# Performance work log

Measured on AMD Instinct MI355X. Metric: run time of the kernel, lower is better.

Reference implementation:

```python
import math
import jax, jax.numpy as jnp
import numpy as np

DIM = 1536
HEADS = 8
DK = 64
DV = 192
NRPF = 192  # num_rel_pos_features, divisible by 6
SEQ = 1536
BATCH = 4
SCALE = DK ** -0.5


def get_positional_embed(n, feature_size):
    # distances in [-(n-1), n-1], length 2n-1
    dist = jnp.arange(-n + 1, n).astype(jnp.float32)
    adist = jnp.abs(dist)[:, None]  # [2n-1, 1]
    f = feature_size // 6  # 3 feature fns, each doubled by sign channel
    # exponential half-life features
    max_range = math.log(n) / math.log(2.0)
    half_life = 2.0 ** jnp.linspace(3.0, max_range, f)[None, :]
    emb_exp = jnp.exp(-math.log(2.0) / half_life * adist)
    # central mask features
    center_widths = (2.0 ** jnp.arange(1, f + 1).astype(jnp.float32) - 1.0)[None, :]
    emb_cm = (center_widths > adist).astype(jnp.float32)
    # gamma pdf features
    stddev = n / (2.0 * f)
    start_mean = n / float(f)
    mean = jnp.linspace(start_mean, float(n), f)[None, :]
    conc = (mean / stddev) ** 2
    rate = mean / stddev ** 2
    log_unnorm = (conc - 1.0) * jnp.log(jnp.maximum(adist, 1e-20)) - rate * adist
    log_norm = jax.scipy.special.gammaln(conc) - conc * jnp.log(rate)
    prob = jnp.exp(log_unnorm - log_norm) + 1e-8
    emb_g = prob / jnp.max(prob, axis=-1, keepdims=True)
    emb = jnp.concatenate([emb_exp, emb_cm, emb_g], axis=-1)  # [2n-1, feat/2]
    return jnp.concatenate([emb, jnp.sign(dist)[:, None] * emb], axis=-1)  # [2n-1, feat]


def relative_shift(x):
    # x: [b, h, n, 2n-1] -> [b, h, n, n] via the Transformer-XL shift trick
    b, h, t1, t2 = x.shape
    x = jnp.concatenate([jnp.zeros_like(x[..., :1]), x], axis=-1)  # [b,h,t1,t2+1]
    x = x.reshape(b, h, t2 + 1, t1)[:, :, 1:, :].reshape(b, h, t1, t2)
    return x[..., : (t2 + 2) // 2]


def layer_norm(x, g, b, eps=1e-5):
    mu = jnp.mean(x, axis=-1, keepdims=True)
    var = jnp.var(x, axis=-1, keepdims=True)
    return (x - mu) * jax.lax.rsqrt(var + eps) * g + b


def setup_inputs() -> dict:
    key = jax.random.key(0)
    ks = jax.random.split(key, 16)
    d, h, dk, dv = DIM, HEADS, DK, DV
    inp = {
        "x": jax.random.normal(ks[0], (BATCH, SEQ, d), dtype=jnp.float32),
        "ln1_g": jnp.ones((d,), jnp.float32),
        "ln1_b": jnp.zeros((d,), jnp.float32),
        "Wq": jax.random.normal(ks[1], (d, h * dk), jnp.float32) / math.sqrt(d),
        "Wk": jax.random.normal(ks[2], (d, h * dk), jnp.float32) / math.sqrt(d),
        "Wv": jax.random.normal(ks[3], (d, h * dv), jnp.float32) / math.sqrt(d),
        "Wo": jax.random.normal(ks[4], (h * dv, d), jnp.float32) / math.sqrt(h * dv),
        "bo": jnp.zeros((d,), jnp.float32),
        "Wrk": jax.random.normal(ks[5], (NRPF, h * dk), jnp.float32) / math.sqrt(NRPF),
        "rel_content_bias": jax.random.normal(ks[6], (1, h, 1, dk), jnp.float32),
        "rel_pos_bias": jax.random.normal(ks[7], (1, h, 1, dk), jnp.float32),
        "ln2_g": jnp.ones((d,), jnp.float32),
        "ln2_b": jnp.zeros((d,), jnp.float32),
        "W1": jax.random.normal(ks[8], (d, 2 * d), jnp.float32) / math.sqrt(d),
        "b1": jnp.zeros((2 * d,), jnp.float32),
        "W2": jax.random.normal(ks[9], (2 * d, d), jnp.float32) / math.sqrt(2 * d),
        "b2": jnp.zeros((d,), jnp.float32),
    }
    return inp


def _attention(x, Wq, Wk, Wv, Wo, bo, Wrk, rel_content_bias, rel_pos_bias):
    b, n, _ = x.shape
    h, dk, dv = HEADS, DK, DV
    q = (x @ Wq).reshape(b, n, h, dk).transpose(0, 2, 1, 3) * SCALE  # [b,h,n,dk]
    k = (x @ Wk).reshape(b, n, h, dk).transpose(0, 2, 1, 3)
    v = (x @ Wv).reshape(b, n, h, dv).transpose(0, 2, 1, 3)
    content_logits = jnp.einsum('bhid,bhjd->bhij', q + rel_content_bias, k)
    positions = get_positional_embed(n, NRPF)  # [2n-1, NRPF]
    rel_k = (positions @ Wrk).reshape(2 * n - 1, h, dk).transpose(1, 0, 2)  # [h,2n-1,dk]
    rel_logits = jnp.einsum('bhid,hjd->bhij', q + rel_pos_bias, rel_k)
    rel_logits = relative_shift(rel_logits)  # [b,h,n,n]
    attn = jax.nn.softmax(content_logits + rel_logits, axis=-1)
    out = jnp.einsum('bhij,bhjd->bhid', attn, v)
    out = out.transpose(0, 2, 1, 3).reshape(b, n, h * dv)
    return out @ Wo + bo


def reference(x, ln1_g, ln1_b, Wq, Wk, Wv, Wo, bo, Wrk, rel_content_bias,
              rel_pos_bias, ln2_g, ln2_b, W1, b1, W2, b2):
    # pre-LN attention with residual
    x = x + _attention(layer_norm(x, ln1_g, ln1_b), Wq, Wk, Wv, Wo, bo, Wrk,
                       rel_content_bias, rel_pos_bias)
    # MLP block (carries its own LayerNorm and residual)
    y = layer_norm(x, ln2_g, ln2_b)
    y = jax.nn.relu(y @ W1 + b1)
    y = y @ W2 + b2
    return y + x
```

## Files before the change

### kernel.cpp

```cpp
#include <hip/hip_runtime.h>
#include <hip/hip_bf16.h>
#include <math.h>

#define SEQN 1536
#define NH 8
#define MROWS 6144
#define NDIST 3071

typedef __attribute__((ext_vector_type(8))) _Float16 f16x8;
typedef __attribute__((ext_vector_type(4))) _Float16 f16x4;
typedef __attribute__((ext_vector_type(4))) float f32x4;

#define MFMAH(a, b, c) __builtin_amdgcn_mfma_f32_16x16x32_f16(a, b, c, 0, 0, 0)

__device__ __forceinline__ void gl_lds16(const void* g, void* l) {
  __builtin_amdgcn_global_load_lds(
      (const __attribute__((address_space(1))) void*)g,
      (__attribute__((address_space(3))) void*)l, 16, 0, 0);
}

__global__ __launch_bounds__(64) void pos_embed_kernel(float* __restrict__ pos) {
  int row = blockIdx.x;
  int j = threadIdx.x;
  if (j >= 32) return;
  float dist = (float)(row - (SEQN - 1));
  float adist = fabsf(dist);
  float sgn = (dist > 0.f) ? 1.f : (dist < 0.f ? -1.f : 0.f);

  const float max_range = 10.58496250072116f;
  float hl = exp2f(3.0f + ((max_range - 3.0f) / 31.0f) * (float)j);
  float e_exp = expf(-0.6931471805599453f / hl * adist);

  float cw = exp2f((float)(j + 1)) - 1.0f;
  float e_cm = (cw > adist) ? 1.0f : 0.0f;

  float mean = 48.0f * (float)(j + 1);
  float tt = mean / 24.0f;
  float conc = tt * tt;
  float rate = mean / 576.0f;
  float log_unnorm = (conc - 1.0f) * logf(fmaxf(adist, 1e-20f)) - rate * adist;
  float log_norm = lgammaf(conc) - conc * logf(rate);
  float prob = expf(log_unnorm - log_norm) + 1e-8f;
  float mx = prob;
  #pragma unroll
  for (int off = 16; off >= 1; off >>= 1)
    mx = fmaxf(mx, __shfl_xor(mx, off, 32));
  float e_g = prob / mx;

  float* o = pos + (size_t)row * 192;
  o[j] = e_exp;        o[32 + j] = e_cm;        o[64 + j] = e_g;
  o[96 + j] = sgn * e_exp; o[128 + j] = sgn * e_cm; o[160 + j] = sgn * e_g;
}

__global__ __launch_bounds__(512) void relk_kernel(
    const float* __restrict__ pos, const float* __restrict__ Wrk,
    const float* __restrict__ pb, _Float16* __restrict__ rk, float* __restrict__ PR) {
  __shared__ float prow[16][192];
  const int d0 = blockIdx.x * 16;
  const int t = threadIdx.x;
  #pragma unroll
  for (int p = 0; p < 6; ++p) {
    int idx = t + p * 512;
    int r = idx / 192, c = idx - r * 192;
    prow[r][c] = pos[(size_t)(d0 + r) * 192 + c];
  }
  __syncthreads();
  float acc[16];
  #pragma unroll
  for (int r = 0; r < 16; ++r) acc[r] = 0.f;
  #pragma unroll 4
  for (int kk = 0; kk < 192; ++kk) {
    float wv = Wrk[(size_t)kk * 512 + t];
    #pragma unroll
    for (int r = 0; r < 16; ++r) acc[r] = fmaf(prow[r][kk], wv, acc[r]);
  }
  #pragma unroll
  for (int r = 0; r < 16; ++r)
    rk[(size_t)(d0 + r) * 512 + t] = (_Float16)acc[r];
  float pbv = pb[t];
  #pragma unroll
  for (int r = 0; r < 16; ++r) {
    float pv = pbv * acc[r];
    #pragma unroll
    for (int off = 32; off >= 1; off >>= 1) pv += __shfl_xor(pv, off);
    if ((t & 63) == 0 && (d0 + r) < NDIST)
      PR[(size_t)(t >> 6) * NDIST + d0 + r] = pv;
  }
}

__global__ __launch_bounds__(256) void ck_kernel(
    const _Float16* __restrict__ Kp, const float* __restrict__ cb,
    float* __restrict__ CK) {
  const int gid = blockIdx.x * 4 + (threadIdx.x >> 6);
  const int lane = threadIdx.x & 63;
  const int row = gid >> 3;
  const int h = gid & 7;
  float kv = (float)Kp[(size_t)row * 512 + h * 64 + lane];
  float pv = cb[h * 64 + lane] * kv;
  #pragma unroll
  for (int off = 32; off >= 1; off >>= 1) pv += __shfl_xor(pv, off);
  if (lane == 0) CK[(size_t)row * 8 + h] = pv;
}

__global__ __launch_bounds__(256) void ln_kernel(
    const float* __restrict__ x, const float* __restrict__ g,
    const float* __restrict__ bta, _Float16* __restrict__ oh) {
  const int row = blockIdx.x;
  const int t = threadIdx.x;
  __shared__ float red[4];
  __shared__ float bc[2];
  const float4* xr = (const float4*)(x + (size_t)row * 1536);
  float4 v0 = xr[t];
  float4 v1 = make_float4(0.f, 0.f, 0.f, 0.f);
  if (t < 128) v1 = xr[256 + t];
  float s = v0.x + v0.y + v0.z + v0.w;
  if (t < 128) s += v1.x + v1.y + v1.z + v1.w;
  #pragma unroll
  for (int off = 32; off >= 1; off >>= 1) s += __shfl_xor(s, off);
  if ((t & 63) == 0) red[t >> 6] = s;
  __syncthreads();
  if (t == 0) bc[0] = (red[0] + red[1] + red[2] + red[3]) * (1.f / 1536.f);
  __syncthreads();
  const float mu = bc[0];
  float d, s2 = 0.f;
  d = v0.x - mu; s2 += d * d; d = v0.y - mu; s2 += d * d;
  d = v0.z - mu; s2 += d * d; d = v0.w - mu; s2 += d * d;
  if (t < 128) {
    d = v1.x - mu; s2 += d * d; d = v1.y - mu; s2 += d * d;
    d = v1.z - mu; s2 += d * d; d = v1.w - mu; s2 += d * d;
  }
  #pragma unroll
  for (int off = 32; off >= 1; off >>= 1) s2 += __shfl_xor(s2, off);
  if ((t & 63) == 0) red[t >> 6] = s2;
  __syncthreads();
  if (t == 0) bc[1] = (red[0] + red[1] + red[2] + red[3]) * (1.f / 1536.f);
  __syncthreads();
  const float inv = rsqrtf(bc[1] + 1e-5f);
  const float4* g4 = (const float4*)g;
  const float4* b4 = (const float4*)bta;
  float4 gg = g4[t], bb = b4[t];
  f16x4 hv;
  hv[0] = (_Float16)((v0.x - mu) * inv * gg.x + bb.x);
  hv[1] = (_Float16)((v0.y - mu) * inv * gg.y + bb.y);
  hv[2] = (_Float16)((v0.z - mu) * inv * gg.z + bb.z);
  hv[3] = (_Float16)((v0.w - mu) * inv * gg.w + bb.w);
  *(f16x4*)(oh + (size_t)row * 1536 + t * 4) = hv;
  if (t < 128) {
    gg = g4[256 + t]; bb = b4[256 + t];
    hv[0] = (_Float16)((v1.x - mu) * inv * gg.x + bb.x);
    hv[1] = (_Float16)((v1.y - mu) * inv * gg.y + bb.y);
    hv[2] = (_Float16)((v1.z - mu) * inv * gg.z + bb.z);
    hv[3] = (_Float16)((v1.w - mu) * inv * gg.w + bb.w);
    *(f16x4*)(oh + (size_t)row * 1536 + 1024 + t * 4) = hv;
  }
}

__global__ __launch_bounds__(256) void convw_kernel(
    const float* __restrict__ W, _Float16* __restrict__ Th,
    int N, int K, int KD, int roff, float scale) {
  __shared__ float tile[32][33];
  const int n0 = blockIdx.x * 32, k0 = blockIdx.y * 32;
  const int t = threadIdx.x;
  const int cr = t >> 5;
  const int cc = t & 31;
  #pragma unroll
  for (int p = 0; p < 4; ++p) {
    int r = cr + p * 8;
    tile[r][cc] = W[(size_t)(k0 + r) * N + n0 + cc];
  }
  __syncthreads();
  #pragma unroll
  for (int p = 0; p < 4; ++p) {
    int r = cr + p * 8;
    float v = tile[cc][r] * scale;
    Th[(size_t)(roff + n0 + r) * KD + k0 + cc] = (_Float16)v;
  }
}

template <int EPI, int BNJ, int MW>
__global__ __launch_bounds__(256, MW) void mgemm_kernel(
    const _Float16* __restrict__ A, const _Float16* __restrict__ B,
    float* __restrict__ C, _Float16* __restrict__ Ch,
    _Float16* __restrict__ Kp, _Float16* __restrict__ Vt,
    const float* __restrict__ bias, const float* __restrict__ res,
    int M, int N, int K) {
  constexpr int BN = BNJ * 32;
  __shared__ _Float16 sm[8192 + BN * 64];
  const int t = threadIdx.x;
  const int lane = t & 63;
  const int w = t >> 6;
  const int wm = w >> 1, wn = w & 1;
  const int slab = (M >> 7) >> 3;
  const int xcd = blockIdx.x & 7;
  const int r = blockIdx.x >> 3;
  const int yt = xcd * slab + (r % slab);
  const int xt = r / slab;
  const int m0 = yt * 128, n0 = xt * BN;

  f32x4 acc[4][BNJ];
  #pragma unroll
  for (int i = 0; i < 4; ++i)
    #pragma unroll
    for (int j = 0; j < BNJ; ++j) acc[i][j] = (f32x4){0.f, 0.f, 0.f, 0.f};

  const int srow = t >> 3;
  const int ssl = t & 7;
  const int ss = ssl ^ (srow & 7);
  const int lr = lane & 15;
  const int g = lane >> 4;
  const int kb = lr & 7;

  for (int k0 = 0; k0 < K; k0 += 64) {
    #pragma unroll
    for (int p = 0; p < 4; ++p) {
      int row = srow + p * 32;
      gl_lds16(A + (size_t)(m0 + row) * K + k0 + ss * 8, &sm[row * 64 + ssl * 8]);
    }
    #pragma unroll
    for (int p = 0; p < BN / 32; ++p) {
      int row = srow + p * 32;
      gl_lds16(B + (size_t)(n0 + row) * K + k0 + ss * 8,
               &sm[8192 + row * 64 + ssl * 8]);
    }
    __syncthreads();
    #pragma unroll
    for (int h2 = 0; h2 < 2; ++h2) {
      const int ksl = ((h2 * 4 + g) ^ kb) * 8;
      f16x8 a[4], b[BNJ];
      #pragma unroll
      for (int i = 0; i < 4; ++i)
        a[i] = *(const f16x8*)(&sm[(wm * 64 + i * 16 + lr) * 64 + ksl]);
      #pragma unroll
      for (int j = 0; j < BNJ; ++j)
        b[j] = *(const f16x8*)(&sm[8192 + (wn * BNJ * 16 + j * 16 + lr) * 64 + ksl]);
      #pragma unroll
      for (int i = 0; i < 4; ++i)
        #pragma unroll
        for (int j = 0; j < BNJ; ++j)
          acc[i][j] = MFMAH(a[i], b[j], acc[i][j]);
    }
    __syncthreads();
  }

  const int lq = lane >> 4;
  #pragma unroll
  for (int i = 0; i < 4; ++i) {
    #pragma unroll
    for (int j = 0; j < BNJ; ++j) {
      const int c0 = n0 + wn * BNJ * 16 + j * 16;
      const int col = c0 + lr;
      const int rbase = m0 + wm * 64 + i * 16 + lq * 4;
      if (EPI == 3) {
        #pragma unroll
        for (int q = 0; q < 4; ++q) {
          size_t o = (size_t)(rbase + q) * N + col;
          C[o] = acc[i][j][q] + bias[col] + res[o];
        }
      } else if (EPI == 2) {
        #pragma unroll
        for (int q = 0; q < 4; ++q) {
          size_t o = (size_t)(rbase + q) * N + col;
          Ch[o] = (_Float16)fmaxf(acc[i][j][q] + bias[col], 0.f);
        }
      } else {
        if (c0 < 512) {
          #pragma unroll
          for (int q = 0; q < 4; ++q)
            Ch[(size_t)(rbase + q) * 512 + col] = (_Float16)acc[i][j][q];
        } else if (c0 < 1024) {
          #pragma unroll
          for (int q = 0; q < 4; ++q)
            Kp[(size_t)(rbase + q) * 512 + (col - 512)] = (_Float16)acc[i][j][q];
        } else {
          int dv = col - 1024;
          int hd = dv / 192;
          int dvh = dv - hd * 192;
          int bb = rbase / 1536;
          int nloc = rbase - bb * 1536;
          f16x4 pk;
          pk[0] = (_Float16)acc[i][j][0];
          pk[1] = (_Float16)acc[i][j][1];
          pk[2] = (_Float16)acc[i][j][2];
          pk[3] = (_Float16)acc[i][j][3];
          *(f16x4*)(Vt + (((size_t)bb * 8 + hd) * 192 + dvh) * 1536 + nloc) = pk;
        }
      }
    }
  }
}

__global__ __launch_bounds__(256, 3) void attn_kernel(
    const _Float16* __restrict__ Qp, const _Float16* __restrict__ Kp,
    const _Float16* __restrict__ Vt, const _Float16* __restrict__ rk,
    const float* __restrict__ PR, const float* __restrict__ CK,
    _Float16* __restrict__ ao) {
  __shared__ _Float16 lds[26752];
  const int id = blockIdx.x;
  const int xcd = id & 7, s = id >> 3;
  const int bh = xcd * 4 + s / 24;
  const int it = s % 24;
  const int b = bh >> 3, h = bh & 7;
  const int t = threadIdx.x;
  const int w = t >> 6;
  const int lane = t & 63;
  const int c15 = lane & 15, g = lane >> 4;
  const int swz = c15 & 7;
  const int vsz = (c15 >> 1) & 3;
  const int qrow0 = it * 64 + w * 16;
  const int rrow0 = 48 - w * 16;
  const int R0 = 1472 - it * 64;

  const int lr = lane >> 3, sl = lane & 7;
  const int ss = sl ^ lr;
  const int ss2 = (lane & 3) ^ ((lane >> 3) & 3);

  f16x8 qh0, qh1;
  {
    size_t qo = ((size_t)(b * SEQN + qrow0 + c15)) * 512 + h * 64 + g * 8;
    qh0 = *(const f16x8*)(Qp + qo);
    qh1 = *(const f16x8*)(Qp + qo + 32);
  }
  f16x8 ones;
  #pragma unroll
  for (int i = 0; i < 8; ++i) ones[i] = (_Float16)1.0f;
  const float* PRrow = PR + (size_t)h * NDIST;
  const float* CKb2 = CK + (size_t)b * SEQN * 8 + h;

  f32x4 acc[13];
  #pragma unroll
  for (int d = 0; d < 13; ++d) acc[d] = (f32x4){0.f, 0.f, 0.f, 0.f};
  float mrun[4];
  #pragma unroll
  for (int q = 0; q < 4; ++q) mrun[q] = -1e30f;

  #define STAGE_KV(J0, KB, VB)                                                   \
    do {                                                                         \
      size_t gk = ((size_t)(b * SEQN + (J0) + w * 8 + lr)) * 512 + h * 64 + ss * 8; \
      gl_lds16(Kp + gk, &lds[(KB) + w * 512]);                                   \
      _Pragma("unroll") for (int p = 0; p < 3; ++p) {                            \
        int rv = w * 48 + p * 16 + (lane >> 2);                                  \
        size_t gv = (((size_t)(b * 8 + h)) * 192 + rv) * SEQN + (J0) + ss2 * 8;  \
        gl_lds16(Vt + gv, &lds[(VB) + (w * 48 + p * 16) * 32]);                  \
      }                                                                          \
    } while (0)

  #define STAGE_R_PRO()                                                          \
    do {                                                                         \
      _Pragma("unroll") for (int p = 0; p < 4; ++p) {                            \
        int rr = w * 32 + p * 8 + lr;                                            \
        size_t gr = ((size_t)(R0 + rr)) * 512 + h * 64 + ss * 8;                 \
        gl_lds16(rk + gr, &lds[16384 + (w * 32 + p * 8) * 64]);                  \
      }                                                                          \
    } while (0)

  #define STAGE_R_INC(REL0)                                                      \
    do {                                                                         \
      int rr = (REL0) + w * 8 + lr;                                              \
      size_t gr = ((size_t)(R0 + rr)) * 512 + h * 64 + ss * 8;                   \
      gl_lds16(rk + gr, &lds[16384 + ((((REL0) + w * 8) & 127)) * 64]);          \
    } while (0)

  #define COMP_T(DST, ETOFF)                                                     \
    do {                                                                         \
      int relrow = (cc32 + rrow0 + (ETOFF) + c15) & 127;                         \
      f16x8 r0_ = *(const f16x8*)(&lds[16384 + relrow * 64 + (g ^ swz) * 8]);    \
      f16x8 r1_ = *(const f16x8*)(&lds[16384 + relrow * 64 + ((4 + g) ^ swz) * 8]); \
      f32x4 tt_ = (f32x4){0.f, 0.f, 0.f, 0.f};                                   \
      tt_ = MFMAH(qh0, r0_, tt_);                                                \
      tt_ = MFMAH(qh1, r1_, tt_);                                                \
      float prv_ = PRrow[dbase + (ETOFF) + c15];                                 \
      _Pragma("unroll") for (int q = 0; q < 4; ++q) tt_[q] += prv_;              \
      DST = tt_;                                                                 \
    } while (0)

  STAGE_KV(0, 0, 4096);
  STAGE_R_PRO();

  f32x4 T0, T1, T2;

  for (int c = 0; c < 48; ++c) {
    const int j0 = c * 32;
    const int cc32 = c * 32;
    const int cur = c & 1;
    const int KB = cur * 2048;
    const int VB = 4096 + cur * 6144;
    __syncthreads();

    if (c < 47) {
      STAGE_KV(j0 + 32, (cur ^ 1) * 2048, 4096 + (cur ^ 1) * 6144);
      if (c >= 1) STAGE_R_INC(cc32 + 96);
    }

    const int dbase = 1520 + j0 - qrow0;
    __builtin_amdgcn_s_setprio(1);
    if (c == 0) {
      COMP_T(T0, 0);
    } else {
      T0 = T2;
    }
    COMP_T(T1, 16);
    COMP_T(T2, 32);
    f32x4 S[2];
    #pragma unroll
    for (int st = 0; st < 2; ++st) {
      int rowK = st * 16 + c15;
      f16x8 kh0 = *(const f16x8*)(&lds[KB + rowK * 64 + (g ^ swz) * 8]);
      f16x8 kh1 = *(const f16x8*)(&lds[KB + rowK * 64 + ((4 + g) ^ swz) * 8]);
      f32x4 ssv = (f32x4){0.f, 0.f, 0.f, 0.f};
      ssv = MFMAH(qh0, kh0, ssv);
      ssv = MFMAH(qh1, kh1, ssv);
      S[st] = ssv;
    }
    __builtin_amdgcn_s_setprio(0);
    float ck0 = CKb2[(size_t)(j0 + c15) * 8];
    float ck1 = CKb2[(size_t)(j0 + 16 + c15) * 8];
    #pragma unroll
    for (int q = 0; q < 4; ++q) {
      int eoff = c15 + 15 - 4 * g - q;
      int src = (lane & 48) | (eoff & 15);
      float t0v = __shfl(T0[q], src);
      float t1v = __shfl(T1[q], src);
      float t2v = __shfl(T2[q], src);
      bool lo = eoff < 16;
      S[0][q] += ck0 + (lo ? t0v : t1v);
      S[1][q] += ck1 + (lo ? t1v : t2v);
    }
    int need = 0;
    #pragma unroll
    for (int st = 0; st < 2; ++st)
      #pragma unroll
      for (int q = 0; q < 4; ++q) need |= (S[st][q] > mrun[q] + 8.0f) ? 1 : 0;
    if (__any(need)) {
      float mx[4];
      #pragma unroll
      for (int q = 0; q < 4; ++q) mx[q] = fmaxf(S[0][q], S[1][q]);
      #pragma unroll
      for (int off = 8; off >= 1; off >>= 1)
        #pragma unroll
        for (int q = 0; q < 4; ++q) mx[q] = fmaxf(mx[q], __shfl_xor(mx[q], off));
      #pragma unroll
      for (int q = 0; q < 4; ++q) {
        float mn = fmaxf(mrun[q], mx[q]);
        float al = __expf(mrun[q] - mn);
        mrun[q] = mn;
        #pragma unroll
        for (int d = 0; d < 13; ++d) acc[d][q] *= al;
      }
    }
    #pragma unroll
    for (int st = 0; st < 2; ++st)
      #pragma unroll
      for (int q = 0; q < 4; ++q)
        lds[24576 + (w * 16 + 4 * g + q) * 34 + st * 16 + c15] =
            (_Float16)__expf(S[st][q] - mrun[q]);

    f16x8 pf = *(const f16x8*)(&lds[24576 + (w * 16 + c15) * 34 + g * 8]);
    __builtin_amdgcn_s_setprio(1);
    #pragma unroll
    for (int d = 0; d < 12; ++d) {
      int rowV = d * 16 + c15;
      f16x8 vf = *(const f16x8*)(&lds[VB + rowV * 32 + (g ^ vsz) * 8]);
      acc[d] = MFMAH(pf, vf, acc[d]);
    }
    acc[12] = MFMAH(pf, ones, acc[12]);
    __builtin_amdgcn_s_setprio(0);
  }

  float rinv[4];
  #pragma unroll
  for (int q = 0; q < 4; ++q) rinv[q] = 1.0f / acc[12][q];
  #pragma unroll
  for (int d = 0; d < 12; ++d) {
    int col = h * 192 + d * 16 + c15;
    #pragma unroll
    for (int q = 0; q < 4; ++q) {
      size_t row = (size_t)(b * SEQN + qrow0 + 4 * g + q);
      ao[row * 1536 + col] = (_Float16)(acc[d][q] * rinv[q]);
    }
  }
  #undef STAGE_KV
  #undef STAGE_R_PRO
  #undef STAGE_R_INC
  #undef COMP_T
}

extern "C" void kernel_launch(void* const* d_in, const int* in_sizes, int n_in,
                              void* d_out, int out_size, void* d_ws, size_t ws_size,
                              hipStream_t stream) {
  (void)in_sizes; (void)n_in; (void)out_size; (void)ws_size;
  const float* x   = (const float*)d_in[0];
  const float* g1  = (const float*)d_in[1];
  const float* be1 = (const float*)d_in[2];
  const float* Wq  = (const float*)d_in[3];
  const float* Wk  = (const float*)d_in[4];
  const float* Wv  = (const float*)d_in[5];
  const float* Wo  = (const float*)d_in[6];
  const float* bo  = (const float*)d_in[7];
  const float* Wrk = (const float*)d_in[8];
  const float* cb  = (const float*)d_in[9];
  const float* pb  = (const float*)d_in[10];
  const float* g2  = (const float*)d_in[11];
  const float* be2 = (const float*)d_in[12];
  const float* W1  = (const float*)d_in[13];
  const float* b1  = (const float*)d_in[14];
  const float* W2  = (const float*)d_in[15];
  const float* b2  = (const float*)d_in[16];
  float* out = (float*)d_out;

  char* B = (char*)d_ws;
  float* pos     = (float*)(B + 0);
  _Float16* rk   = (_Float16*)(B + 2359296);
  float* PRb     = (float*)(B + 5505024);
  float* CKb     = (float*)(B + 5603328);
  _Float16* xn   = (_Float16*)(B + 5799936);
  _Float16* Wb   = (_Float16*)(B + 24674304);
  _Float16* Qp   = (_Float16*)(B + 34111488);
  _Float16* Kp   = (_Float16*)(B + 40402944);
  _Float16* Vtp  = (_Float16*)(B + 46694400);
  _Float16* ao   = (_Float16*)(B + 65568768);
  float* x2      = (float*)(B + 84443136);
  _Float16* h1   = (_Float16*)(B + 122191872);

  pos_embed_kernel<<<NDIST, 64, 0, stream>>>(pos);
  relk_kernel<<<192, 512, 0, stream>>>(pos, Wrk, pb, rk, PRb);
  ln_kernel<<<MROWS, 256, 0, stream>>>(x, g1, be1, xn);
  convw_kernel<<<dim3(16, 48), 256, 0, stream>>>(Wq, Wb, 512, 1536, 1536, 0, 0.125f);
  convw_kernel<<<dim3(16, 48), 256, 0, stream>>>(Wk, Wb, 512, 1536, 1536, 512, 1.0f);
  convw_kernel<<<dim3(48, 48), 256, 0, stream>>>(Wv, Wb, 1536, 1536, 1536, 1024, 1.0f);
  mgemm_kernel<4, 4, 4><<<960, 256, 0, stream>>>(
      xn, Wb, nullptr, Qp, Kp, Vtp, nullptr, nullptr, MROWS, 2560, 1536);
  ck_kernel<<<MROWS * 2, 256, 0, stream>>>(Kp, cb, CKb);
  attn_kernel<<<768, 256, 0, stream>>>(Qp, Kp, Vtp, rk, PRb, CKb, ao);
  convw_kernel<<<dim3(48, 48), 256, 0, stream>>>(Wo, Wb, 1536, 1536, 1536, 0, 1.0f);
  mgemm_kernel<3, 3, 4><<<768, 256, 0, stream>>>(
      ao, Wb, x2, nullptr, nullptr, nullptr, bo, x, MROWS, 1536, 1536);
  ln_kernel<<<MROWS, 256, 0, stream>>>(x2, g2, be2, xn);
  convw_kernel<<<dim3(96, 48), 256, 0, stream>>>(W1, Wb, 3072, 1536, 1536, 0, 1.0f);
  mgemm_kernel<2, 6, 3><<<768, 256, 0, stream>>>(
      xn, Wb, nullptr, h1, nullptr, nullptr, b1, nullptr, MROWS, 3072, 1536);
  convw_kernel<<<dim3(48, 96), 256, 0, stream>>>(W2, Wb, 1536, 3072, 3072, 0, 1.0f);
  mgemm_kernel<3, 3, 4><<<768, 256, 0, stream>>>(
      h1, Wb, out, nullptr, nullptr, nullptr, b2, x2, MROWS, 1536, 3072);
}
```

Baseline: 427.1 us.

## Fuse content-bias key dot into QKV GEMM epilogue and unroll attention loop

Removes the separate ck_kernel and computes the per-row content-bias dot product with K inside the QKV GEMM epilogue, using cross-lane shuffles over the fp32 accumulators. The attention main loop is unrolled by two with compile-time double-buffer offsets and incrementing global pointers, which cuts per-iteration address arithmetic. The cost is one fewer launch and one fewer read of K. The CK value now comes from unrounded fp32 accumulators rather than fp16-rounded K, which changes numerics slightly. The unrolled loop may also raise register pressure.

```diff
diff --git a/kernel.cpp b/kernel.cpp
--- a/kernel.cpp
+++ b/kernel.cpp
@@ -86,20 +86,6 @@
     if ((t & 63) == 0 && (d0 + r) < NDIST)
       PR[(size_t)(t >> 6) * NDIST + d0 + r] = pv;
   }
-}
-
-__global__ __launch_bounds__(256) void ck_kernel(
-    const _Float16* __restrict__ Kp, const float* __restrict__ cb,
-    float* __restrict__ CK) {
-  const int gid = blockIdx.x * 4 + (threadIdx.x >> 6);
-  const int lane = threadIdx.x & 63;
-  const int row = gid >> 3;
-  const int h = gid & 7;
-  float kv = (float)Kp[(size_t)row * 512 + h * 64 + lane];
-  float pv = cb[h * 64 + lane] * kv;
-  #pragma unroll
-  for (int off = 32; off >= 1; off >>= 1) pv += __shfl_xor(pv, off);
-  if (lane == 0) CK[(size_t)row * 8 + h] = pv;
 }
 
 __global__ __launch_bounds__(256) void ln_kernel(
@@ -181,7 +167,7 @@
 __global__ __launch_bounds__(256, MW) void mgemm_kernel(
     const _Float16* __restrict__ A, const _Float16* __restrict__ B,
     float* __restrict__ C, _Float16* __restrict__ Ch,
-    _Float16* __restrict__ Kp, _Float16* __restrict__ Vt,
+    _Float16* __restrict__ Kp, _Float16* __restrict__ Vt, float* __restrict__ CKo,
     const float* __restrict__ bias, const float* __restrict__ res,
     int M, int N, int K) {
   constexpr int BN = BNJ * 32;
@@ -287,6 +273,27 @@
       }
     }
   }
+
+  if (EPI == 4) {
+    const int cw0 = n0 + wn * 64;
+    if (cw0 >= 512 && cw0 < 1024) {
+      const int hh = (cw0 - 512) >> 6;
+      float cbv[4];
+      #pragma unroll
+      for (int j = 0; j < 4; ++j) cbv[j] = bias[cw0 - 512 + j * 16 + lr];
+      #pragma unroll
+      for (int i = 0; i < 4; ++i)
+        #pragma unroll
+        for (int q = 0; q < 4; ++q) {
+          float v = acc[i][0][q] * cbv[0] + acc[i][1][q] * cbv[1] +
+                    acc[i][2][q] * cbv[2] + acc[i][3][q] * cbv[3];
+          #pragma unroll
+          for (int off = 8; off >= 1; off >>= 1) v += __shfl_xor(v, off);
+          if (lr == 0)
+            CKo[(size_t)(m0 + wm * 64 + i * 16 + lq * 4 + q) * 8 + hh] = v;
+        }
+    }
+  }
 }
 
 __global__ __launch_bounds__(256, 3) void attn_kernel(
@@ -323,8 +330,18 @@
   f16x8 ones;
   #pragma unroll
   for (int i = 0; i < 8; ++i) ones[i] = (_Float16)1.0f;
-  const float* PRrow = PR + (size_t)h * NDIST;
-  const float* CKb2 = CK + (size_t)b * SEQN * 8 + h;
+
+  const int klA = c15 * 64 + ((g ^ swz)) * 8;
+  const int klB = c15 * 64 + (((4 + g) ^ swz)) * 8;
+  const int vl  = c15 * 32 + ((g ^ vsz)) * 8;
+  const int pwr = 24576 + (w * 16 + 4 * g) * 34 + c15;
+  const int pfr = 24576 + (w * 16 + c15) * 34 + g * 8;
+
+  const _Float16* kg = Kp + ((size_t)(b * SEQN) + 32 + w * 8 + lr) * 512 + h * 64 + ss * 8;
+  const _Float16* vg = Vt + (((size_t)(b * 8 + h)) * 192 + w * 48 + (lane >> 2)) * SEQN + 32 + ss2 * 8;
+  const _Float16* rg = rk + ((size_t)(R0 + 96) + w * 8 + lr) * 512 + h * 64 + ss * 8;
+  const float* prg = PR + (size_t)h * NDIST + 1520 - qrow0 + c15;
+  const float* ckg = CK + (size_t)b * SEQN * 8 + h + c15 * 8;
 
   f32x4 acc[13];
   #pragma unroll
@@ -333,138 +350,124 @@
   #pragma unroll
   for (int q = 0; q < 4; ++q) mrun[q] = -1e30f;
 
-  #define STAGE_KV(J0, KB, VB)                                                   \
-    do {                                                                         \
-      size_t gk = ((size_t)(b * SEQN + (J0) + w * 8 + lr)) * 512 + h * 64 + ss * 8; \
-      gl_lds16(Kp + gk, &lds[(KB) + w * 512]);                                   \
-      _Pragma("unroll") for (int p = 0; p < 3; ++p) {                            \
-        int rv = w * 48 + p * 16 + (lane >> 2);                                  \
-        size_t gv = (((size_t)(b * 8 + h)) * 192 + rv) * SEQN + (J0) + ss2 * 8;  \
-        gl_lds16(Vt + gv, &lds[(VB) + (w * 48 + p * 16) * 32]);                  \
-      }                                                                          \
+  {
+    size_t gk = ((size_t)(b * SEQN) + w * 8 + lr) * 512 + h * 64 + ss * 8;
+    gl_lds16(Kp + gk, &lds[w * 512]);
+    #pragma unroll
+    for (int p = 0; p < 3; ++p) {
+      size_t gv = (((size_t)(b * 8 + h)) * 192 + w * 48 + p * 16 + (lane >> 2)) * SEQN + ss2 * 8;
+      gl_lds16(Vt + gv, &lds[4096 + (w * 48 + p * 16) * 32]);
+    }
+    #pragma unroll
+    for (int p = 0; p < 4; ++p) {
+      int rr = w * 32 + p * 8 + lr;
+      size_t gr = ((size_t)(R0 + rr)) * 512 + h * 64 + ss * 8;
+      gl_lds16(rk + gr, &lds[16384 + (w * 32 + p * 8) * 64]);
+    }
+  }
+
+  f32x4 T0, T1, T2;
+
+  #define COMP_T(DST, ETOFF)                                                    \
+    do {                                                                        \
+      int relrow = (cc32 + rrow0 + (ETOFF) + c15) & 127;                        \
+      f16x8 r0_ = *(const f16x8*)(&lds[16384 + relrow * 64 + ((g ^ swz)) * 8]); \
+      f16x8 r1_ = *(const f16x8*)(&lds[16384 + relrow * 64 + (((4 + g) ^ swz)) * 8]); \
+      f32x4 tt_ = (f32x4){0.f, 0.f, 0.f, 0.f};                                  \
+      tt_ = MFMAH(qh0, r0_, tt_);                                               \
+      tt_ = MFMAH(qh1, r1_, tt_);                                               \
+      float prv_ = prg[(ETOFF)];                                                \
+      _Pragma("unroll") for (int q = 0; q < 4; ++q) tt_[q] += prv_;             \
+      DST = tt_;                                                                \
     } while (0)
 
-  #define STAGE_R_PRO()                                                          \
-    do {                                                                         \
-      _Pragma("unroll") for (int p = 0; p < 4; ++p) {                            \
-        int rr = w * 32 + p * 8 + lr;                                            \
-        size_t gr = ((size_t)(R0 + rr)) * 512 + h * 64 + ss * 8;                 \
-        gl_lds16(rk + gr, &lds[16384 + (w * 32 + p * 8) * 64]);                  \
-      }                                                                          \
-    } while (0)
-
-  #define STAGE_R_INC(REL0)                                                      \
-    do {                                                                         \
-      int rr = (REL0) + w * 8 + lr;                                              \
-      size_t gr = ((size_t)(R0 + rr)) * 512 + h * 64 + ss * 8;                   \
-      gl_lds16(rk + gr, &lds[16384 + ((((REL0) + w * 8) & 127)) * 64]);          \
-    } while (0)
-
-  #define COMP_T(DST, ETOFF)                                                     \
-    do {                                                                         \
-      int relrow = (cc32 + rrow0 + (ETOFF) + c15) & 127;                         \
-      f16x8 r0_ = *(const f16x8*)(&lds[16384 + relrow * 64 + (g ^ swz) * 8]);    \
-      f16x8 r1_ = *(const f16x8*)(&lds[16384 + relrow * 64 + ((4 + g) ^ swz) * 8]); \
-      f32x4 tt_ = (f32x4){0.f, 0.f, 0.f, 0.f};                                   \
-      tt_ = MFMAH(qh0, r0_, tt_);                                                \
-      tt_ = MFMAH(qh1, r1_, tt_);                                                \
-      float prv_ = PRrow[dbase + (ETOFF) + c15];                                 \
-      _Pragma("unroll") for (int q = 0; q < 4; ++q) tt_[q] += prv_;              \
-      DST = tt_;                                                                 \
-    } while (0)
-
-  STAGE_KV(0, 0, 4096);
-  STAGE_R_PRO();
-
-  f32x4 T0, T1, T2;
-
-  for (int c = 0; c < 48; ++c) {
-    const int j0 = c * 32;
-    const int cc32 = c * 32;
-    const int cur = c & 1;
-    const int KB = cur * 2048;
-    const int VB = 4096 + cur * 6144;
-    __syncthreads();
-
-    if (c < 47) {
-      STAGE_KV(j0 + 32, (cur ^ 1) * 2048, 4096 + (cur ^ 1) * 6144);
-      if (c >= 1) STAGE_R_INC(cc32 + 96);
-    }
-
-    const int dbase = 1520 + j0 - qrow0;
-    __builtin_amdgcn_s_setprio(1);
-    if (c == 0) {
-      COMP_T(T0, 0);
-    } else {
-      T0 = T2;
-    }
-    COMP_T(T1, 16);
-    COMP_T(T2, 32);
-    f32x4 S[2];
-    #pragma unroll
-    for (int st = 0; st < 2; ++st) {
-      int rowK = st * 16 + c15;
-      f16x8 kh0 = *(const f16x8*)(&lds[KB + rowK * 64 + (g ^ swz) * 8]);
-      f16x8 kh1 = *(const f16x8*)(&lds[KB + rowK * 64 + ((4 + g) ^ swz) * 8]);
-      f32x4 ssv = (f32x4){0.f, 0.f, 0.f, 0.f};
-      ssv = MFMAH(qh0, kh0, ssv);
-      ssv = MFMAH(qh1, kh1, ssv);
-      S[st] = ssv;
-    }
-    __builtin_amdgcn_s_setprio(0);
-    float ck0 = CKb2[(size_t)(j0 + c15) * 8];
-    float ck1 = CKb2[(size_t)(j0 + 16 + c15) * 8];
-    #pragma unroll
-    for (int q = 0; q < 4; ++q) {
-      int eoff = c15 + 15 - 4 * g - q;
-      int src = (lane & 48) | (eoff & 15);
-      float t0v = __shfl(T0[q], src);
-      float t1v = __shfl(T1[q], src);
-      float t2v = __shfl(T2[q], src);
-      bool lo = eoff < 16;
-      S[0][q] += ck0 + (lo ? t0v : t1v);
-      S[1][q] += ck1 + (lo ? t1v : t2v);
-    }
-    int need = 0;
-    #pragma unroll
-    for (int st = 0; st < 2; ++st)
-      #pragma unroll
-      for (int q = 0; q < 4; ++q) need |= (S[st][q] > mrun[q] + 8.0f) ? 1 : 0;
-    if (__any(need)) {
-      float mx[4];
-      #pragma unroll
-      for (int q = 0; q < 4; ++q) mx[q] = fmaxf(S[0][q], S[1][q]);
-      #pragma unroll
-      for (int off = 8; off >= 1; off >>= 1)
-        #pragma unroll
-        for (int q = 0; q < 4; ++q) mx[q] = fmaxf(mx[q], __shfl_xor(mx[q], off));
-      #pragma unroll
-      for (int q = 0; q < 4; ++q) {
-        float mn = fmaxf(mrun[q], mx[q]);
-        float al = __expf(mrun[q] - mn);
-        mrun[q] = mn;
-        #pragma unroll
-        for (int d = 0; d < 13; ++d) acc[d][q] *= al;
-      }
-    }
-    #pragma unroll
-    for (int st = 0; st < 2; ++st)
-      #pragma unroll
-      for (int q = 0; q < 4; ++q)
-        lds[24576 + (w * 16 + 4 * g + q) * 34 + st * 16 + c15] =
-            (_Float16)__expf(S[st][q] - mrun[q]);
-
-    f16x8 pf = *(const f16x8*)(&lds[24576 + (w * 16 + c15) * 34 + g * 8]);
-    __builtin_amdgcn_s_setprio(1);
-    #pragma unroll
-    for (int d = 0; d < 12; ++d) {
-      int rowV = d * 16 + c15;
-      f16x8 vf = *(const f16x8*)(&lds[VB + rowV * 32 + (g ^ vsz) * 8]);
-      acc[d] = MFMAH(pf, vf, acc[d]);
-    }
-    acc[12] = MFMAH(pf, ones, acc[12]);
-    __builtin_amdgcn_s_setprio(0);
-  }
+  #define CHUNK_BODY(CIDX, P)                                                   \
+  {                                                                             \
+    const int c = (CIDX);                                                       \
+    const int cc32 = c * 32;                                                    \
+    constexpr int KB = (P) * 2048;                                              \
+    constexpr int VB = 4096 + (P) * 6144;                                       \
+    constexpr int KBn = (1 - (P)) * 2048;                                       \
+    constexpr int VBn = 4096 + (1 - (P)) * 6144;                                \
+    __syncthreads();  \
+    if (c < 47) {                                                               \
+      gl_lds16(kg, &lds[KBn + w * 512]);                                        \
+      gl_lds16(vg, &lds[VBn + (w * 48) * 32]);                                  \
+      gl_lds16(vg + (size_t)16 * SEQN, &lds[VBn + (w * 48 + 16) * 32]);         \
+      gl_lds16(vg + (size_t)32 * SEQN, &lds[VBn + (w * 48 + 32) * 32]);         \
+      if (c >= 1) {                                                             \
+        int dr = ((cc32 + 96 + w * 8) & 127) * 64;                              \
+        gl_lds16(rg, &lds[16384 + dr]);                                         \
+      }                                                                         \
+    }                                                                           \
+    __builtin_amdgcn_s_setprio(1);                                              \
+    if (c == 0) { COMP_T(T0, 0); } else { T0 = T2; }                            \
+    COMP_T(T1, 16);                                                             \
+    COMP_T(T2, 32);                                                             \
+    f32x4 S[2];                                                                 \
+    _Pragma("unroll") for (int st = 0; st < 2; ++st) {                          \
+      f16x8 kh0 = *(const f16x8*)(&lds[KB + st * 1024 + klA]);                  \
+      f16x8 kh1 = *(const f16x8*)(&lds[KB + st * 1024 + klB]);                  \
+      f32x4 ssv = (f32x4){0.f, 0.f, 0.f, 0.f};                                  \
+      ssv = MFMAH(qh0, kh0, ssv);                                               \
+      ssv = MFMAH(qh1, kh1, ssv);                                               \
+      S[st] = ssv;                                                              \
+    }                                                                           \
+    __builtin_amdgcn_s_setprio(0);                                              \
+    float ck0 = ckg[0];                                                         \
+    float ck1 = ckg[128];                                                       \
+    _Pragma("unroll") for (int q = 0; q < 4; ++q) {                             \
+      int eoff = c15 + 15 - 4 * g - q;                                          \
+      int src = (lane & 48) | (eoff & 15);                                      \
+      float t0v = __shfl(T0[q], src);                                           \
+      float t1v = __shfl(T1[q], src);                                           \
+      float t2v = __shfl(T2[q], src);                                           \
+      bool lo = eoff < 16;                                                      \
+      S[0][q] += ck0 + (lo ? t0v : t1v);                                        \
+      S[1][q] += ck1 + (lo ? t1v : t2v);                                        \
+    }                                                                           \
+    int need = 0;                                                               \
+    _Pragma("unroll") for (int st = 0; st < 2; ++st)                            \
+      _Pragma("unroll") for (int q = 0; q < 4; ++q)                             \
+        need |= (S[st][q] > mrun[q] + 8.0f) ? 1 : 0;                            \
+    if (__any(need)) {                                                          \
+      float mx[4];                                                              \
+      _Pragma("unroll") for (int q = 0; q < 4; ++q)                             \
+        mx[q] = fmaxf(S[0][q], S[1][q]);                                        \
+      _Pragma("unroll") for (int off = 8; off >= 1; off >>= 1)                  \
+        _Pragma("unroll") for (int q = 0; q < 4; ++q)                           \
+          mx[q] = fmaxf(mx[q], __shfl_xor(mx[q], off));                         \
+      _Pragma("unroll") for (int q = 0; q < 4; ++q) {                           \
+        float mn = fmaxf(mrun[q], mx[q]);                                       \
+        float al = __expf(mrun[q] - mn);                                        \
+        mrun[q] = mn;                                                           \
+        _Pragma("unroll") for (int d = 0; d < 13; ++d) acc[d][q] *= al;         \
+      }                                                                         \
+    }                                                                           \
+    _Pragma("unroll") for (int st = 0; st < 2; ++st)                            \
+      _Pragma("unroll") for (int q = 0; q < 4; ++q)                             \
+        lds[pwr + q * 34 + st * 16] = (_Float16)__expf(S[st][q] - mrun[q]);     \
+    f16x8 pf = *(const f16x8*)(&lds[pfr]);                                      \
+    __builtin_amdgcn_s_setprio(1);                                              \
+    _Pragma("unroll") for (int d = 0; d < 12; ++d) {                            \
+      f16x8 vf = *(const f16x8*)(&lds[VB + d * 512 + vl]);                      \
+      acc[d] = MFMAH(pf, vf, acc[d]);                                           \
+    }                                                                           \
+    acc[12] = MFMAH(pf, ones, acc[12]);                                         \
+    __builtin_amdgcn_s_setprio(0);                                              \
+    kg += 32 * 512;                                                             \
+    vg += 32;                                                                   \
+    rg += 32 * 512;                                                             \
+    prg += 32;                                                                  \
+    ckg += 256;                                                                 \
+  }
+
+  for (int cc = 0; cc < 48; cc += 2) {
+    CHUNK_BODY(cc, 0);
+    CHUNK_BODY(cc + 1, 1);
+  }
+  #undef CHUNK_BODY
+  #undef COMP_T
 
   float rinv[4];
   #pragma unroll
@@ -478,10 +481,6 @@
       ao[row * 1536 + col] = (_Float16)(acc[d][q] * rinv[q]);
     }
   }
-  #undef STAGE_KV
-  #undef STAGE_R_PRO
-  #undef STAGE_R_INC
-  #undef COMP_T
 }
 
 extern "C" void kernel_launch(void* const* d_in, const int* in_sizes, int n_in,
@@ -528,17 +527,16 @@
   convw_kernel<<<dim3(16, 48), 256, 0, stream>>>(Wk, Wb, 512, 1536, 1536, 512, 1.0f);
   convw_kernel<<<dim3(48, 48), 256, 0, stream>>>(Wv, Wb, 1536, 1536, 1536, 1024, 1.0f);
   mgemm_kernel<4, 4, 4><<<960, 256, 0, stream>>>(
-      xn, Wb, nullptr, Qp, Kp, Vtp, nullptr, nullptr, MROWS, 2560, 1536);
-  ck_kernel<<<MROWS * 2, 256, 0, stream>>>(Kp, cb, CKb);
+      xn, Wb, nullptr, Qp, Kp, Vtp, CKb, cb, nullptr, MROWS, 2560, 1536);
   attn_kernel<<<768, 256, 0, stream>>>(Qp, Kp, Vtp, rk, PRb, CKb, ao);
   convw_kernel<<<dim3(48, 48), 256, 0, stream>>>(Wo, Wb, 1536, 1536, 1536, 0, 1.0f);
   mgemm_kernel<3, 3, 4><<<768, 256, 0, stream>>>(
-      ao, Wb, x2, nullptr, nullptr, nullptr, bo, x, MROWS, 1536, 1536);
+      ao, Wb, x2, nullptr, nullptr, nullptr, nullptr, bo, x, MROWS, 1536, 1536);
   ln_kernel<<<MROWS, 256, 0, stream>>>(x2, g2, be2, xn);
   convw_kernel<<<dim3(96, 48), 256, 0, stream>>>(W1, Wb, 3072, 1536, 1536, 0, 1.0f);
   mgemm_kernel<2, 6, 3><<<768, 256, 0, stream>>>(
-      xn, Wb, nullptr, h1, nullptr, nullptr, b1, nullptr, MROWS, 3072, 1536);
+      xn, Wb, nullptr, h1, nullptr, nullptr, nullptr, b1, nullptr, MROWS, 3072, 1536);
   convw_kernel<<<dim3(48, 96), 256, 0, stream>>>(W2, Wb, 1536, 3072, 3072, 0, 1.0f);
   mgemm_kernel<3, 3, 4><<<768, 256, 0, stream>>>(
-      h1, Wb, out, nullptr, nullptr, nullptr, b2, x2, MROWS, 1536, 3072);
-}
+      h1, Wb, out, nullptr, nullptr, nullptr, nullptr, b2, x2, MROWS, 1536, 3072);
+}
```

After: 420.2 us. No clear change (-1.6%).
